# Kernel optimization log

Hardware: AMD Instinct MI355X
Metric: run time of the kernel (lower is better)

Reference implementation:

```python
import jax, jax.numpy as jnp
import numpy as np

EMBED_DIM = 1024
SEQ_LEN = 2048
BATCH = 8


def setup_inputs() -> dict:
    key = jax.random.key(0)
    ks = jax.random.split(key, 7)
    s = 1.0 / np.sqrt(EMBED_DIM)
    x = jax.random.normal(ks[0], (BATCH, SEQ_LEN, EMBED_DIM), dtype=jnp.float32)
    # torch nn.Linear stores weight as [out, in]; init U(-1/sqrt(in), 1/sqrt(in))
    Wq = jax.random.uniform(ks[1], (EMBED_DIM, EMBED_DIM), jnp.float32, -s, s)
    bq = jax.random.uniform(ks[2], (EMBED_DIM,), jnp.float32, -s, s)
    Wk = jax.random.uniform(ks[3], (EMBED_DIM, EMBED_DIM), jnp.float32, -s, s)
    bk = jax.random.uniform(ks[4], (EMBED_DIM,), jnp.float32, -s, s)
    Wv = jax.random.uniform(ks[5], (EMBED_DIM, EMBED_DIM), jnp.float32, -s, s)
    bv = jax.random.uniform(ks[6], (EMBED_DIM,), jnp.float32, -s, s)
    return {"x": x, "Wq": Wq, "bq": bq, "Wk": Wk, "bk": bk, "Wv": Wv, "bv": bv}


def reference(x, Wq, bq, Wk, bk, Wv, bv):
    # Linear projections (torch Linear: x @ W.T + b)
    q = jnp.einsum("bse,oe->bso", x, Wq) + bq
    k = jnp.einsum("bse,oe->bso", x, Wk) + bk
    v = jnp.einsum("bse,oe->bso", x, Wv) + bv
    scale = 1.0 / jnp.sqrt(jnp.float32(EMBED_DIM))
    sims = jnp.einsum("bqe,bke->bqk", q, k) * scale  # [B, S, S]
    causal = jnp.tril(jnp.ones((SEQ_LEN, SEQ_LEN), dtype=bool))
    masked = jnp.where(causal, sims, jnp.float32(-1e9))
    attn = jax.nn.softmax(masked, axis=2)
    return jnp.einsum("bqk,bke->bqe", attn, v)
```

## Files before the change

kernel.cpp:

```cpp
#include <hip/hip_runtime.h>
#include <hip/hip_bf16.h>
#include <stdint.h>
#include <math.h>

#define DEVI __device__ __forceinline__

typedef __attribute__((ext_vector_type(8))) __bf16    bf16x8;
typedef __attribute__((ext_vector_type(8))) _Float16  f16x8;
typedef __attribute__((ext_vector_type(4))) float     f32x4;

constexpr int BM = 128, BN = 128, BK = 64;

DEVI unsigned int pack2(float a, float b) {
  unsigned short ha = __builtin_bit_cast(unsigned short, __float2bfloat16(a));
  unsigned short hb = __builtin_bit_cast(unsigned short, __float2bfloat16(b));
  return (unsigned int)ha | ((unsigned int)hb << 16);
}

__global__ __launch_bounds__(256) void k_cvt_all(const float* __restrict__ x,
                                                 const float* __restrict__ Wq,
                                                 const float* __restrict__ Wk,
                                                 const float* __restrict__ Wv,
                                                 __hip_bfloat16* __restrict__ xb,
                                                 __hip_bfloat16* __restrict__ Wqb,
                                                 __hip_bfloat16* __restrict__ Wkb,
                                                 __hip_bfloat16* __restrict__ Wvb) {
  int i = blockIdx.x * 256 + threadIdx.x;
  const float* src;
  __hip_bfloat16* dst;
  int k;
  if (i < 4194304) {
    src = x; dst = xb; k = i;
  } else {
    int j = i - 4194304;
    int w = j >> 18;
    k = j & 262143;
    src = (w == 0) ? Wq : (w == 1) ? Wk : Wv;
    dst = (w == 0) ? Wqb : (w == 1) ? Wkb : Wvb;
  }
  float4 f = ((const float4*)src)[k];
  uint2 u;
  u.x = pack2(f.x, f.y);
  u.y = pack2(f.z, f.w);
  ((uint2*)dst)[k] = u;
}

DEVI void stage_tile(const __hip_bfloat16* gbase, int ld, unsigned short* lds, int tid) {
#pragma unroll
  for (int j = 0; j < 4; ++j) {
    int g   = j * 256 + tid;
    int row = g >> 3;
    int cp  = g & 7;
    int c   = cp ^ (row & 7);
    const __hip_bfloat16* src = gbase + (size_t)row * ld + c * 8;
    unsigned short* dst = lds + (size_t)(j * 256 + (tid & ~63)) * 8;
    __builtin_amdgcn_global_load_lds((__attribute__((address_space(1))) void*)(src),
                                     (__attribute__((address_space(3))) void*)(dst),
                                     16, 0, 0);
  }
}

DEVI bf16x8 read_frag(const unsigned short* lds, int row, int kcol) {
  int c  = kcol >> 3;
  int cp = c ^ (row & 7);
  return *(const bf16x8*)(lds + row * 64 + cp * 8);
}

DEVI void gemm_core(unsigned short* sA, unsigned short* sB,
                    const __hip_bfloat16* A0, int lda,
                    const __hip_bfloat16* B0, int ldb,
                    int ktiles, f32x4 (&acc)[4][4]) {
  const int tid  = threadIdx.x;
  const int lane = tid & 63;
  const int wid  = tid >> 6;
  const int quad = lane >> 4;
  const int lr   = lane & 15;
  const int wm   = (wid >> 1) * 64;
  const int wn   = (wid & 1) * 64;
  const f32x4 Z = {0.f, 0.f, 0.f, 0.f};
#pragma unroll
  for (int i = 0; i < 4; ++i)
#pragma unroll
    for (int j = 0; j < 4; ++j) acc[i][j] = Z;

  for (int kt = 0; kt < ktiles; ++kt) {
    stage_tile(A0 + kt * BK, lda, sA, tid);
    stage_tile(B0 + kt * BK, ldb, sB, tid);
    __syncthreads();
#pragma unroll
    for (int ks = 0; ks < BK; ks += 32) {
      bf16x8 af[4], bfr[4];
#pragma unroll
      for (int t = 0; t < 4; ++t) af[t]  = read_frag(sA, wm + t * 16 + lr, ks + quad * 8);
#pragma unroll
      for (int t = 0; t < 4; ++t) bfr[t] = read_frag(sB, wn + t * 16 + lr, ks + quad * 8);
#pragma unroll
      for (int i = 0; i < 4; ++i)
#pragma unroll
        for (int j = 0; j < 4; ++j)
          acc[i][j] = __builtin_amdgcn_mfma_f32_16x16x32_bf16(af[i], bfr[j], acc[i][j], 0, 0, 0);
    }
    __syncthreads();
  }
}

__global__ __launch_bounds__(256, 4) void k_proj_qkv(const __hip_bfloat16* __restrict__ X,
                                                     const __hip_bfloat16* __restrict__ Wq,
                                                     const __hip_bfloat16* __restrict__ Wk,
                                                     const __hip_bfloat16* __restrict__ Wv,
                                                     const float* __restrict__ bq,
                                                     const float* __restrict__ bk,
                                                     const float* __restrict__ bv,
                                                     __hip_bfloat16* __restrict__ Q,
                                                     __hip_bfloat16* __restrict__ Kp,
                                                     __hip_bfloat16* __restrict__ Vt) {
  __shared__ unsigned short sA[BM * BK];
  __shared__ unsigned short sB[BN * BK];
  const int id = blockIdx.x;
  const int w  = id >> 10;
  const int i2 = id & 1023;
  const int mt = ((i2 & 7) << 4) | ((i2 >> 3) & 15);
  const int nt = i2 >> 7;
  const int m0 = mt * BM;
  const int n0 = nt * BN;

  const __hip_bfloat16* W = (w == 0) ? Wq : (w == 1) ? Wk : Wv;
  const float* bias       = (w == 0) ? bq : (w == 1) ? bk : bv;

  f32x4 acc[4][4];
  gemm_core(sA, sB, X + (size_t)m0 * 1024, 1024, W + (size_t)n0 * 1024, 1024, 16, acc);

  const int tid = threadIdx.x, lane = tid & 63, wid = tid >> 6;
  const int quad = lane >> 4, lr = lane & 15;
  const int wm = (wid >> 1) * 64, wn = (wid & 1) * 64;
  float bvv[4];
#pragma unroll
  for (int j = 0; j < 4; ++j) bvv[j] = bias[n0 + wn + j * 16 + lr];

  if (w != 2) {
    __hip_bfloat16* C = (w == 0) ? Q : Kp;
#pragma unroll
    for (int i = 0; i < 4; ++i)
#pragma unroll
      for (int j = 0; j < 4; ++j) {
        int n = n0 + wn + j * 16 + lr;
#pragma unroll
        for (int r = 0; r < 4; ++r) {
          int m = m0 + wm + i * 16 + quad * 4 + r;
          C[(size_t)m * 1024 + n] = __float2bfloat16(acc[i][j][r] + bvv[j]);
        }
      }
  } else {
    const int b = m0 >> 11;
    __hip_bfloat16* Cb = Vt + ((size_t)b << 21);
    const int sb = (m0 & 2047) + wm;
#pragma unroll
    for (int i = 0; i < 4; ++i)
#pragma unroll
      for (int j = 0; j < 4; ++j) {
        int n  = n0 + wn + j * 16 + lr;
        int s0 = sb + i * 16 + quad * 4;
        uint2 u;
        u.x = pack2(acc[i][j][0] + bvv[j], acc[i][j][1] + bvv[j]);
        u.y = pack2(acc[i][j][2] + bvv[j], acc[i][j][3] + bvv[j]);
        *(uint2*)(Cb + (size_t)n * 2048 + s0) = u;
      }
  }
}

__global__ __launch_bounds__(256, 4) void k_scores(const __hip_bfloat16* __restrict__ Q,
                                                   const __hip_bfloat16* __restrict__ Kmat,
                                                   _Float16* __restrict__ S,
                                                   int b0, int zmask, int zshift) {
  __shared__ unsigned short sA[BM * BK];
  __shared__ unsigned short sB[BN * BK];
  const int id = blockIdx.x;
  const int z = id & zmask;
  const int b = b0 + z;
  const int i = id >> zshift;
  int qt = (int)((sqrtf(8.f * (float)i + 1.f) - 1.f) * 0.5f);
  while ((qt + 1) * (qt + 2) / 2 <= i) ++qt;
  while (qt * (qt + 1) / 2 > i) --qt;
  const int kt = i - qt * (qt + 1) / 2;

  const int m0 = qt * BM, n0 = kt * BN;
  f32x4 acc[4][4];
  const __hip_bfloat16* A0 = Q    + ((size_t)b << 21) + (size_t)m0 * 1024;
  const __hip_bfloat16* B0 = Kmat + ((size_t)b << 21) + (size_t)n0 * 1024;
  gemm_core(sA, sB, A0, 1024, B0, 1024, 16, acc);

  _Float16* Sb = S + ((size_t)z << 22);
  const int tid = threadIdx.x, lane = tid & 63, wid = tid >> 6;
  const int quad = lane >> 4, lr = lane & 15;
  const int wm = (wid >> 1) * 64, wn = (wid & 1) * 64;
#pragma unroll
  for (int i2 = 0; i2 < 4; ++i2)
#pragma unroll
    for (int j = 0; j < 4; ++j) {
      int n = n0 + wn + j * 16 + lr;
#pragma unroll
      for (int r = 0; r < 4; ++r) {
        int m = m0 + wm + i2 * 16 + quad * 4 + r;
        Sb[(size_t)m * 2048 + n] = (_Float16)(acc[i2][j][r] * 0.03125f);
      }
    }
}

__global__ __launch_bounds__(256) void k_softmax(_Float16* __restrict__ S) {
  const int row = blockIdx.x;
  const int q = row & 2047;
  _Float16* srow = S + ((size_t)row << 11);
  const int t = threadIdx.x;
  const int k0 = t << 3;

  float v[8];
  float mx = -1e30f;
  if (k0 <= q) {
    f16x8 h = ((const f16x8*)srow)[t];
#pragma unroll
    for (int i = 0; i < 8; ++i) {
      float f = (float)h[i];
      v[i] = (k0 + i <= q) ? f : -1e30f;
      mx = fmaxf(mx, v[i]);
    }
  } else {
#pragma unroll
    for (int i = 0; i < 8; ++i) v[i] = -1e30f;
  }
#pragma unroll
  for (int off = 32; off > 0; off >>= 1) mx = fmaxf(mx, __shfl_xor(mx, off));
  __shared__ float rmax[4], rsum[4];
  if ((t & 63) == 0) rmax[t >> 6] = mx;
  __syncthreads();
  mx = fmaxf(fmaxf(rmax[0], rmax[1]), fmaxf(rmax[2], rmax[3]));

  float e[8], s = 0.f;
#pragma unroll
  for (int i = 0; i < 8; ++i) { e[i] = __expf(v[i] - mx); s += e[i]; }
#pragma unroll
  for (int off = 32; off > 0; off >>= 1) s += __shfl_xor(s, off);
  if ((t & 63) == 0) rsum[t >> 6] = s;
  __syncthreads();
  s = rsum[0] + rsum[1] + rsum[2] + rsum[3];
  const float inv = 1.0f / s;

  bf16x8 o;
#pragma unroll
  for (int i = 0; i < 8; ++i) o[i] = (__bf16)(e[i] * inv);
  ((bf16x8*)srow)[t] = o;
}

DEVI void pv_one(unsigned short* sA, unsigned short* sB,
                 const __hip_bfloat16* P, const __hip_bfloat16* VtB,
                 float* Cb, int qt, int nt) {
  const int m0 = qt * BM, n0 = nt * BN;
  const int ktiles = 2 * qt + 2;
  f32x4 acc[4][4];
  gemm_core(sA, sB, P + (size_t)m0 * 2048, 2048, VtB + (size_t)n0 * 2048, 2048, ktiles, acc);

  const int tid = threadIdx.x, lane = tid & 63, wid = tid >> 6;
  const int quad = lane >> 4, lr = lane & 15;
  const int wm = (wid >> 1) * 64, wn = (wid & 1) * 64;
#pragma unroll
  for (int i = 0; i < 4; ++i)
#pragma unroll
    for (int j = 0; j < 4; ++j) {
      int n = n0 + wn + j * 16 + lr;
#pragma unroll
      for (int r = 0; r < 4; ++r) {
        int m = m0 + wm + i * 16 + quad * 4 + r;
        Cb[(size_t)m * 1024 + n] = acc[i][j][r];
      }
    }
}

__global__ __launch_bounds__(256, 4) void k_pv(const _Float16* __restrict__ Sbase,
                                               const __hip_bfloat16* __restrict__ Vt,
                                               float* __restrict__ out,
                                               int b0, int zmask, int zshift) {
  __shared__ unsigned short sA[BM * BK];
  __shared__ unsigned short sB[BN * BK];
  const int id = blockIdx.x;
  const int z = id & zmask;
  const int b = b0 + z;
  const int r2 = id >> zshift;
  const int nt = r2 & 7;
  const int p  = (r2 >> 3) & 7;
  const __hip_bfloat16* P   = (const __hip_bfloat16*)(Sbase + ((size_t)z << 22));
  const __hip_bfloat16* VtB = Vt + ((size_t)b << 21);
  float* Cb = out + ((size_t)b << 21);
  pv_one(sA, sB, P, VtB, Cb, 15 - p, nt);
  pv_one(sA, sB, P, VtB, Cb, p, nt);
}

extern "C" void kernel_launch(void* const* d_in, const int* in_sizes, int n_in,
                              void* d_out, int out_size, void* d_ws, size_t ws_size,
                              hipStream_t stream) {
  const float* x  = (const float*)d_in[0];
  const float* Wq = (const float*)d_in[1];
  const float* bq = (const float*)d_in[2];
  const float* Wk = (const float*)d_in[3];
  const float* bk = (const float*)d_in[4];
  const float* Wv = (const float*)d_in[5];
  const float* bv = (const float*)d_in[6];
  float* out = (float*)d_out;

  char* ws = (char*)d_ws;
  const size_t MB32 = (size_t)33554432;
  const size_t MB64 = (size_t)67108864;

  __hip_bfloat16 *xb, *Wqb, *Wkb, *Wvb, *Q, *Kp, *Vt;
  _Float16* S;
  int G;
  if (ws_size >= (size_t)174063616) {
    S   = (_Float16*)(ws);
    xb  = (__hip_bfloat16*)(ws);
    Wqb = (__hip_bfloat16*)(ws + MB64);
    Wkb = (__hip_bfloat16*)(ws + MB64 + 2097152);
    Wvb = (__hip_bfloat16*)(ws + MB64 + 4194304);
    Q   = (__hip_bfloat16*)(ws + MB64 + 6291456);
    Kp  = (__hip_bfloat16*)(ws + MB64 + 6291456 + MB32);
    Vt  = (__hip_bfloat16*)(ws + MB64 + 6291456 + 2 * MB32);
    G = 8;
  } else {
    S   = (_Float16*)(ws);
    xb  = (__hip_bfloat16*)(ws);
    Wqb = (__hip_bfloat16*)(ws + MB32);
    Wkb = (__hip_bfloat16*)(ws + MB32 + 2097152);
    Wvb = (__hip_bfloat16*)(ws + MB32 + 4194304);
    Q   = (__hip_bfloat16*)(ws + MB32 + 6291456);
    Kp  = (__hip_bfloat16*)(ws + 2 * MB32 + 6291456);
    Vt  = (__hip_bfloat16*)(ws + 3 * MB32 + 6291456);
    G = 4;
  }
  const int zmask  = G - 1;
  const int zshift = (G == 8) ? 3 : 2;

  dim3 blk(256);
  k_cvt_all<<<dim3(19456), blk, 0, stream>>>(x, Wq, Wk, Wv, xb, Wqb, Wkb, Wvb);
  k_proj_qkv<<<dim3(3072), blk, 0, stream>>>(xb, Wqb, Wkb, Wvb, bq, bk, bv, Q, Kp, Vt);

  for (int b0 = 0; b0 < 8; b0 += G) {
    k_scores <<<dim3(G * 136),  blk, 0, stream>>>(Q, Kp, S, b0, zmask, zshift);
    k_softmax<<<dim3(G * 2048), blk, 0, stream>>>(S);
    k_pv     <<<dim3(G * 64),   blk, 0, stream>>>(S, Vt, out, b0, zmask, zshift);
  }
}
```

Measured before the change: 335.5 us.

## Rewrite QKV projection as 256x256 tile GEMM with double-buffered LDS pipeline

Replaces the 128x128 single-buffered QKV projection GEMM with a 512-thread kernel that computes 256x256 tiles. It double-buffers 128KB of LDS with staged half-tile async global-to-LDS loads, interleaved with four MFMA phases per k-step. The loop uses explicit barriers, waitcnt control and s_setprio to raise MFMA priority. The larger tiles improve data reuse and the overlap hides load latency. In exchange it needs many more registers and restricts occupancy to 2 blocks per CU, with a small grid of 768 blocks.

```diff
diff --git a/kernel.cpp b/kernel.cpp
--- a/kernel.cpp
+++ b/kernel.cpp
@@ -60,6 +60,21 @@
   }
 }
 
+DEVI void stage_half(const __hip_bfloat16* gbase, int ld, unsigned short* lds, int tid) {
+#pragma unroll
+  for (int j = 0; j < 2; ++j) {
+    int g   = j * 512 + tid;
+    int row = g >> 3;
+    int cp  = g & 7;
+    int c   = cp ^ (row & 7);
+    const __hip_bfloat16* src = gbase + (size_t)row * ld + c * 8;
+    unsigned short* dst = lds + (size_t)(j * 512 + (tid & ~63)) * 8;
+    __builtin_amdgcn_global_load_lds((__attribute__((address_space(1))) void*)(src),
+                                     (__attribute__((address_space(3))) void*)(dst),
+                                     16, 0, 0);
+  }
+}
+
 DEVI bf16x8 read_frag(const unsigned short* lds, int row, int kcol) {
   int c  = kcol >> 3;
   int cp = c ^ (row & 7);
@@ -104,61 +119,157 @@
   }
 }
 
-__global__ __launch_bounds__(256, 4) void k_proj_qkv(const __hip_bfloat16* __restrict__ X,
-                                                     const __hip_bfloat16* __restrict__ Wq,
-                                                     const __hip_bfloat16* __restrict__ Wk,
-                                                     const __hip_bfloat16* __restrict__ Wv,
-                                                     const float* __restrict__ bq,
-                                                     const float* __restrict__ bk,
-                                                     const float* __restrict__ bv,
-                                                     __hip_bfloat16* __restrict__ Q,
-                                                     __hip_bfloat16* __restrict__ Kp,
-                                                     __hip_bfloat16* __restrict__ Vt) {
-  __shared__ unsigned short sA[BM * BK];
-  __shared__ unsigned short sB[BN * BK];
+DEVI void phase_in_lgkm() {
+  __builtin_amdgcn_s_barrier();
+  asm volatile("s_waitcnt lgkmcnt(0)" ::: "memory");
+  __builtin_amdgcn_sched_barrier(0);
+}
+DEVI void phase_in() {
+  __builtin_amdgcn_s_barrier();
+  __builtin_amdgcn_sched_barrier(0);
+}
+DEVI void phase_out() {
+  __builtin_amdgcn_sched_barrier(0);
+  __builtin_amdgcn_s_barrier();
+}
+
+#define MFMA16(R0, AF, BF)                                                        \
+  _Pragma("unroll") for (int i = 0; i < 4; ++i)                                   \
+  _Pragma("unroll") for (int j = 0; j < 4; ++j)                                   \
+    acc[(R0) + i][j] =                                                            \
+        __builtin_amdgcn_mfma_f32_16x16x32_bf16(AF[i], BF[j], acc[(R0) + i][j], 0, 0, 0);
+
+__global__ __launch_bounds__(512, 2) void k_proj_qkv2(const __hip_bfloat16* __restrict__ X,
+                                                      const __hip_bfloat16* __restrict__ Wq,
+                                                      const __hip_bfloat16* __restrict__ Wk,
+                                                      const __hip_bfloat16* __restrict__ Wv,
+                                                      const float* __restrict__ bq,
+                                                      const float* __restrict__ bk,
+                                                      const float* __restrict__ bv,
+                                                      __hip_bfloat16* __restrict__ Q,
+                                                      __hip_bfloat16* __restrict__ Kp,
+                                                      __hip_bfloat16* __restrict__ Vt) {
+  __shared__ unsigned short lds[65536];
+
   const int id = blockIdx.x;
-  const int w  = id >> 10;
-  const int i2 = id & 1023;
-  const int mt = ((i2 & 7) << 4) | ((i2 >> 3) & 15);
-  const int nt = i2 >> 7;
-  const int m0 = mt * BM;
-  const int n0 = nt * BN;
-
-  const __hip_bfloat16* W = (w == 0) ? Wq : (w == 1) ? Wk : Wv;
-  const float* bias       = (w == 0) ? bq : (w == 1) ? bk : bv;
-
-  f32x4 acc[4][4];
-  gemm_core(sA, sB, X + (size_t)m0 * 1024, 1024, W + (size_t)n0 * 1024, 1024, 16, acc);
-
-  const int tid = threadIdx.x, lane = tid & 63, wid = tid >> 6;
-  const int quad = lane >> 4, lr = lane & 15;
-  const int wm = (wid >> 1) * 64, wn = (wid & 1) * 64;
+  const int wg = (id & 7) * 96 + (id >> 3);
+  const int mt = wg & 63;
+  const int nt = (wg >> 6) & 3;
+  const int w  = wg >> 8;
+  const int m0 = mt * 256;
+  const int n0 = nt * 256;
+
+  const __hip_bfloat16* W    = (w == 0) ? Wq : (w == 1) ? Wk : Wv;
+  const float*          bias = (w == 0) ? bq : (w == 1) ? bk : bv;
+  const __hip_bfloat16* Ab = X + (size_t)m0 * 1024;
+  const __hip_bfloat16* Bb = W + (size_t)n0 * 1024;
+
+  const int tid  = threadIdx.x;
+  const int lane = tid & 63;
+  const int wid  = tid >> 6;
+  const int quad = lane >> 4;
+  const int lr   = lane & 15;
+  const int widm = wid >> 2;
+  const int widn = wid & 3;
+  const int br0  = (widn & 1) * 64;
+
+  f32x4 acc[8][4];
+  const f32x4 Z = {0.f, 0.f, 0.f, 0.f};
+#pragma unroll
+  for (int i = 0; i < 8; ++i)
+#pragma unroll
+    for (int j = 0; j < 4; ++j) acc[i][j] = Z;
+
+  stage_half(Ab,               1024, lds + 0,            tid);
+  stage_half(Ab + 131072,      1024, lds + 8192,         tid);
+  stage_half(Bb,               1024, lds + 16384,        tid);
+  stage_half(Bb + 131072,      1024, lds + 24576,        tid);
+  stage_half(Ab + 64,          1024, lds + 32768,        tid);
+  stage_half(Ab + 131072 + 64, 1024, lds + 32768 + 8192, tid);
+  asm volatile("s_waitcnt vmcnt(0)" ::: "memory");
+  __builtin_amdgcn_sched_barrier(0);
+  __builtin_amdgcn_s_barrier();
+
+  for (int t = 0; t < 16; ++t) {
+    unsigned short* cur = lds + (t & 1) * 32768;
+    unsigned short* nxt = lds + ((t + 1) & 1) * 32768;
+    const unsigned short* Ar = cur + widm * 8192;
+    const unsigned short* Br = cur + 16384 + (widn >> 1) * 8192;
+
+    bf16x8 a0k0[4], a0k1[4], a1k0[4], a1k1[4], b0f[4], b1f[4];
+
+#pragma unroll
+    for (int i = 0; i < 4; ++i) {
+      a0k0[i] = read_frag(Ar, i * 16 + lr, quad * 8);
+      a0k1[i] = read_frag(Ar, i * 16 + lr, 32 + quad * 8);
+    }
+#pragma unroll
+    for (int j = 0; j < 4; ++j) b0f[j] = read_frag(Br, br0 + j * 16 + lr, quad * 8);
+    if (t < 15) stage_half(Bb + (t + 1) * 64, 1024, nxt + 16384, tid);
+    phase_in_lgkm();
+    __builtin_amdgcn_s_setprio(1);
+    MFMA16(0, a0k0, b0f);
+    __builtin_amdgcn_s_setprio(0);
+    phase_out();
+
+#pragma unroll
+    for (int i = 0; i < 4; ++i) {
+      a1k0[i] = read_frag(Ar, 64 + i * 16 + lr, quad * 8);
+      a1k1[i] = read_frag(Ar, 64 + i * 16 + lr, 32 + quad * 8);
+    }
+#pragma unroll
+    for (int j = 0; j < 4; ++j) b1f[j] = read_frag(Br, br0 + j * 16 + lr, 32 + quad * 8);
+    if (t < 15) stage_half(Bb + 131072 + (t + 1) * 64, 1024, nxt + 24576, tid);
+    phase_in_lgkm();
+    __builtin_amdgcn_s_setprio(1);
+    MFMA16(4, a1k0, b0f);
+    __builtin_amdgcn_s_setprio(0);
+    phase_out();
+
+    if (t < 14) stage_half(Ab + (t + 2) * 64, 1024, cur + 0, tid);
+    phase_in();
+    __builtin_amdgcn_s_setprio(1);
+    MFMA16(0, a0k1, b1f);
+    __builtin_amdgcn_s_setprio(0);
+    phase_out();
+
+    if (t < 14) stage_half(Ab + 131072 + (t + 2) * 64, 1024, cur + 8192, tid);
+    if (t < 14) asm volatile("s_waitcnt vmcnt(4)" ::: "memory");
+    else        asm volatile("s_waitcnt vmcnt(0)" ::: "memory");
+    __builtin_amdgcn_sched_barrier(0);
+    phase_in();
+    __builtin_amdgcn_s_setprio(1);
+    MFMA16(4, a1k1, b1f);
+    __builtin_amdgcn_s_setprio(0);
+    phase_out();
+  }
+
   float bvv[4];
 #pragma unroll
-  for (int j = 0; j < 4; ++j) bvv[j] = bias[n0 + wn + j * 16 + lr];
+  for (int j = 0; j < 4; ++j) bvv[j] = bias[n0 + widn * 64 + j * 16 + lr];
 
   if (w != 2) {
     __hip_bfloat16* C = (w == 0) ? Q : Kp;
 #pragma unroll
-    for (int i = 0; i < 4; ++i)
+    for (int i = 0; i < 8; ++i)
 #pragma unroll
       for (int j = 0; j < 4; ++j) {
-        int n = n0 + wn + j * 16 + lr;
+        int n = n0 + widn * 64 + j * 16 + lr;
 #pragma unroll
         for (int r = 0; r < 4; ++r) {
-          int m = m0 + wm + i * 16 + quad * 4 + r;
+          int m = m0 + widm * 128 + i * 16 + quad * 4 + r;
           C[(size_t)m * 1024 + n] = __float2bfloat16(acc[i][j][r] + bvv[j]);
         }
       }
   } else {
     const int b = m0 >> 11;
     __hip_bfloat16* Cb = Vt + ((size_t)b << 21);
-    const int sb = (m0 & 2047) + wm;
-#pragma unroll
-    for (int i = 0; i < 4; ++i)
+    const int sb = (m0 & 2047) + widm * 128;
+#pragma unroll
+    for (int i = 0; i < 8; ++i)
 #pragma unroll
       for (int j = 0; j < 4; ++j) {
-        int n  = n0 + wn + j * 16 + lr;
+        int n  = n0 + widn * 64 + j * 16 + lr;
         int s0 = sb + i * 16 + quad * 4;
         uint2 u;
         u.x = pack2(acc[i][j][0] + bvv[j], acc[i][j][1] + bvv[j]);
@@ -338,7 +449,7 @@
 
   dim3 blk(256);
   k_cvt_all<<<dim3(19456), blk, 0, stream>>>(x, Wq, Wk, Wv, xb, Wqb, Wkb, Wvb);
-  k_proj_qkv<<<dim3(3072), blk, 0, stream>>>(xb, Wqb, Wkb, Wvb, bq, bk, bv, Q, Kp, Vt);
+  k_proj_qkv2<<<dim3(768), dim3(512), 0, stream>>>(xb, Wqb, Wkb, Wvb, bq, bk, bv, Q, Kp, Vt);
 
   for (int b0 = 0; b0 < 8; b0 += G) {
     k_scores <<<dim3(G * 136),  blk, 0, stream>>>(Q, Kp, S, b0, zmask, zshift);
```

Result: slower. 360.0 us (+7.3%).
